# Kernel tuning notes

Measured on AMD Instinct MI355X. Metric: run time of the kernel, lower is better.

The kernel has to match this reference:

```python
import jax, jax.numpy as jnp
import numpy as np

B, C_IN, C_OUT, H, K = 64, 64, 128, 1855, 6


def setup_inputs() -> dict:
    key = jax.random.key(0)
    k1, k2, k3, k4 = jax.random.split(key, 4)
    x = jax.random.normal(k1, (B, C_IN, H), dtype=jnp.float32)
    # neighbor table [H, K]; valid indices first, -1 padding at the end
    neighbors = jax.random.randint(k2, (H, K), 0, H)
    n_boundary = H // 10
    neighbors = neighbors.at[:n_boundary, K - 2:].set(-1)
    weight_center = jax.random.normal(k3, (C_OUT, C_IN), dtype=jnp.float32) / np.sqrt(C_IN).astype(np.float32)
    weight_neighbors = jax.random.normal(k4, (C_OUT, C_IN, K), dtype=jnp.float32) / np.sqrt(C_IN * K).astype(np.float32)
    bias = jnp.zeros((C_OUT,), dtype=jnp.float32)
    return {
        "x": x,
        "neighbors": neighbors,
        "weight_center": weight_center,
        "weight_neighbors": weight_neighbors,
        "bias": bias,
    }


def reference(x, neighbors, weight_center, weight_neighbors, bias):
    # x: [B, C_in, H]; neighbors: [H, K] with -1 = invalid (valid-first ordering)
    mask = neighbors >= 0                               # [H, K]
    idx = jnp.where(mask, neighbors, 0)                 # safe gather indices
    gathered = x[:, :, idx] * mask.astype(x.dtype)[None, None, :, :]  # [B, C_in, H, K]
    center = jnp.einsum('bch,oc->boh', x, weight_center)              # [B, C_out, H]
    neigh = jnp.einsum('bchk,ock->boh', gathered, weight_neighbors)   # [B, C_out, H]
    counts = (1 + mask.sum(axis=-1)).astype(x.dtype)                  # [H]
    return (center + neigh) / counts[None, None, :] + bias[None, :, None]
```

## Files before the change

### kernel.cpp

```cpp
#include <hip/hip_runtime.h>
#include <stdint.h>

typedef __bf16 bf16x8 __attribute__((ext_vector_type(8)));
typedef float floatx4 __attribute__((ext_vector_type(4)));
typedef float floatx4u __attribute__((ext_vector_type(4), aligned(4)));
typedef unsigned int u32x4 __attribute__((ext_vector_type(4)));
typedef unsigned short u16;
typedef unsigned int u32;

#define CIN   64
#define COUT  128
#define H_    1855
#define KNB   6
#define KTOT  448
#define NSTEPS 14

#define HROW   2064
#define HBUFSZ 33024

#define WP_OFF     ((size_t)H_ * 4096 * 2)
#define CINV_OFF   (WP_OFF + (size_t)COUT * KTOT * 2)
#define ZERO_OFF   (CINV_OFF + 7424)
#define SRCOFF_OFF (ZERO_OFF + 1024)
#define INVOFF 0xFFFFFFFFu

#define PIN4(v) asm volatile("" : "+v"(v))

typedef __attribute__((address_space(1))) unsigned int as1_u32;
typedef __attribute__((address_space(3))) unsigned int as3_u32;
static __device__ __forceinline__ void ld16_to_lds(const void* g, void* l) {
    __builtin_amdgcn_global_load_lds((const as1_u32*)g, (as3_u32*)l, 16, 0, 0);
}

static __device__ inline u16 f32_to_bf16(float f) {
    u32 u = __float_as_uint(f);
    u32 r = (u + 0x7FFFu + ((u >> 16) & 1u)) >> 16;
    return (u16)r;
}

__global__ __launch_bounds__(256) void k_prep(const float* __restrict__ x,
                                              const float* __restrict__ wc,
                                              const float* __restrict__ wn,
                                              const int* __restrict__ nbr,
                                              u16* __restrict__ xt3,
                                              u16* __restrict__ wp,
                                              float* __restrict__ cInvG,
                                              u32* __restrict__ zeroPg,
                                              u32* __restrict__ srcOff) {
    int tid = threadIdx.x;
    if (blockIdx.y == 64) {
        for (int tg = blockIdx.x * 256 + tid; tg < COUT * KTOT; tg += 29 * 256) {
            if (tg < 128) zeroPg[tg] = 0u;
            if (tg < H_) {
                int cnt = 1;
#pragma unroll
                for (int j = 0; j < KNB; ++j) cnt += (nbr[tg * KNB + j] >= 0) ? 1 : 0;
                cInvG[tg] = 1.0f / (float)cnt;
            }
            if (tg < H_ * 8) {
                int h = tg >> 3, s = tg & 7;
                u32 e;
                if (s == 0) e = (u32)h * 8192u;
                else if (s <= 6) {
                    int n = nbr[h * KNB + (s - 1)];
                    e = (n >= 0) ? (u32)n * 8192u : INVOFF;
                } else e = INVOFF;
                srcOff[tg] = e;
            }
            int o = tg / KTOT;
            int rem = tg - o * KTOT;
            int s = rem >> 6, c = rem & 63;
            float v = (s == 0) ? wc[o * CIN + c]
                               : wn[(o * CIN + c) * KNB + (s - 1)];
            wp[tg] = f32_to_bf16(v);
        }
        return;
    }
    __shared__ u32 t32[64][34];
    int h0  = blockIdx.x * 64;
    int bc0 = blockIdx.y * 64;
    int lh = tid & 15;
    int rq = tid >> 4;
    bool safe = (h0 + 64 <= H_);
#pragma unroll
    for (int it = 0; it < 2; ++it) {
        int rp = it * 16 + rq;
        size_t r0 = (size_t)(bc0 + rp * 2) * H_;
        size_t r1 = r0 + H_;
        int h = h0 + lh * 4;
        u32 p[4];
        if (safe) {
            floatx4u f0 = *(const floatx4u*)(x + r0 + h);
            floatx4u f1 = *(const floatx4u*)(x + r1 + h);
#pragma unroll
            for (int j = 0; j < 4; ++j)
                p[j] = (u32)f32_to_bf16(f0[j]) | ((u32)f32_to_bf16(f1[j]) << 16);
        } else {
#pragma unroll
            for (int j = 0; j < 4; ++j) {
                int hh = h + j;
                u16 a = 0, b = 0;
                if (hh < H_) { a = f32_to_bf16(x[r0 + hh]); b = f32_to_bf16(x[r1 + hh]); }
                p[j] = (u32)a | ((u32)b << 16);
            }
        }
#pragma unroll
        for (int j = 0; j < 4; ++j) t32[lh * 4 + j][rp] = p[j];
    }
    __syncthreads();
    int bg = tid & 7;
    int hb = tid >> 3;
#pragma unroll
    for (int ii = 0; ii < 2; ++ii) {
        int hl = ii * 32 + hb;
        int hh = h0 + hl;
        uint2 qa = *(const uint2*)&t32[hl][bg * 4];
        uint2 qb = *(const uint2*)&t32[hl][bg * 4 + 2];
        u32x4 q = {qa.x, qa.y, qb.x, qb.y};
        if (hh < H_)
            *(u32x4*)(xt3 + (size_t)hh * 4096 + bc0 + bg * 8) = q;
    }
}

__global__ __launch_bounds__(256, 2) void k_main(const u16* __restrict__ xt3,
                                                 const u16* __restrict__ wp,
                                                 const float* __restrict__ bias,
                                                 const float* __restrict__ cInvG,
                                                 const u32* __restrict__ srcOff,
                                                 float* __restrict__ out) {
    __shared__ __align__(16) char LDS[2 * HBUFSZ];

    int tid  = threadIdx.x;
    int gbl  = blockIdx.x;
    int bq   = gbl & 15;
    int hs   = gbl >> 4;
    int b0   = bq * 4;
    int h0   = hs * 64;

    int lane = tid & 63;
    int wave = tid >> 6;
    int col  = lane & 15;
    int quad = lane >> 4;
    int m0w  = wave * 32;
    int lane16 = lane & 15;
    int ssub = lane >> 4;
    int bl   = lane16 >> 3;
    int chunk = lane16 & 7;

    const char* xb = (const char*)xt3;

    u32x4 afrag[2][NSTEPS];
#pragma unroll
    for (int mt = 0; mt < 2; ++mt) {
        int o = m0w + mt * 16 + col;
#pragma unroll
        for (int kk = 0; kk < NSTEPS; ++kk)
            afrag[mt][kk] = *(const u32x4*)(wp + o * KTOT + kk * 32 + quad * 8);
    }
#pragma unroll
    for (int mt = 0; mt < 2; ++mt)
#pragma unroll
        for (int kk = 0; kk < NSTEPS; ++kk)
            PIN4(afrag[mt][kk]);

    float biasv[2][4];
#pragma unroll
    for (int mt = 0; mt < 2; ++mt)
#pragma unroll
        for (int r = 0; r < 4; ++r)
            biasv[mt][r] = bias[m0w + mt * 16 + quad * 4 + r];

    float icv[4];
#pragma unroll
    for (int t = 0; t < 4; ++t) {
        int hic = h0 + t * 16 + col;
        icv[t] = cInvG[hic < H_ ? hic : 0];
    }

    u32 colOff = (u32)((b0 + bl) * 128 + chunk * 16);
    u32 zOff   = (u32)ZERO_OFF + (u32)(lane16 * 16);
    u32 offs[4][2][4];
#pragma unroll
    for (int t = 0; t < 4; ++t)
#pragma unroll
        for (int hf = 0; hf < 2; ++hf)
#pragma unroll
            for (int i = 0; i < 4; ++i) {
                int hh = h0 + t * 16 + wave * 4 + i;
                int s  = hf * 4 + ssub;
                u32 e = (hh < H_) ? srcOff[hh * 8 + s] : INVOFF;
                offs[t][hf][i] = (e == INVOFF) ? zOff : (e + colOff);
            }

    int rb = col * HROW + quad * 16;
    char* buf0 = LDS;
    char* buf1 = LDS + HBUFSZ;
    bool bnd = (hs == 28);

#define SGH(t, hf, bufp) do {                                                 \
    _Pragma("unroll")                                                         \
    for (int _j = 0; _j < 8; ++_j) {                                          \
        int _hl = _j >> 1, _bh = _j & 1;                                      \
        ld16_to_lds(xb + offs[t][hf][_hl] + _bh * 256,                        \
                    (bufp) + (wave * 4 + _hl) * HROW + _bh * 1024);           \
    }                                                                         \
} while (0)

#define CA(accv, bufp) do {              \
    _Pragma("unroll") for (int _m = 0; _m < 2; ++_m)                          \
    _Pragma("unroll") for (int _n = 0; _n < 4; ++_n)                          \
        accv[_m][_n] = (floatx4){0.0f, 0.0f, 0.0f, 0.0f};                     \
    __builtin_amdgcn_s_setprio(1);                                            \
    _Pragma("unroll")                                                         \
    for (int kk = 0; kk < 8; ++kk) {                                          \
        int _ko = (kk >> 1) * 256 + (kk & 1) * 64;                            \
        bf16x8 a0 = __builtin_bit_cast(bf16x8, afrag[0][kk]);                 \
        bf16x8 a1 = __builtin_bit_cast(bf16x8, afrag[1][kk]);                 \
        _Pragma("unroll")                                                     \
        for (int _n = 0; _n < 4; ++_n) {                                      \
            bf16x8 bf = *(const bf16x8*)((bufp) + rb + (_n >> 1) * 1024       \
                                         + (_n & 1) * 128 + _ko);             \
            accv[0][_n] = __builtin_amdgcn_mfma_f32_16x16x32_bf16(a0, bf, accv[0][_n], 0, 0, 0); \
            accv[1][_n] = __builtin_amdgcn_mfma_f32_16x16x32_bf16(a1, bf, accv[1][_n], 0, 0, 0); \
        }                                                                     \
    }                                                                         \
    __builtin_amdgcn_s_setprio(0);                                            \
} while (0)

#define CB(accv, bufp) do {            \
    __builtin_amdgcn_s_setprio(1);                                            \
    _Pragma("unroll")                                                         \
    for (int kk = 8; kk < 14; ++kk) {                                         \
        int _k2 = kk - 8;                                                     \
        int _ko = (_k2 >> 1) * 256 + (_k2 & 1) * 64;                          \
        bf16x8 a0 = __builtin_bit_cast(bf16x8, afrag[0][kk]);                 \
        bf16x8 a1 = __builtin_bit_cast(bf16x8, afrag[1][kk]);                 \
        _Pragma("unroll")                                                     \
        for (int _n = 0; _n < 4; ++_n) {                                      \
            bf16x8 bf = *(const bf16x8*)((bufp) + rb + (_n >> 1) * 1024       \
                                         + (_n & 1) * 128 + _ko);             \
            accv[0][_n] = __builtin_amdgcn_mfma_f32_16x16x32_bf16(a0, bf, accv[0][_n], 0, 0, 0); \
            accv[1][_n] = __builtin_amdgcn_mfma_f32_16x16x32_bf16(a1, bf, accv[1][_n], 0, 0, 0); \
        }                                                                     \
    }                                                                         \
    __builtin_amdgcn_s_setprio(0);                                            \
} while (0)

#define EPI(t, accv, BND) do {                                                \
    int _h = h0 + (t) * 16 + col;                                             \
    float _ic = icv[t];                                                       \
    bool _hv = !(BND) || (_h < H_);                                           \
    _Pragma("unroll") for (int _n = 0; _n < 4; ++_n)                          \
    _Pragma("unroll") for (int _m = 0; _m < 2; ++_m)                          \
    _Pragma("unroll") for (int _r = 0; _r < 4; ++_r) {                        \
        int _o = m0w + _m * 16 + quad * 4 + _r;                               \
        float _v = accv[_m][_n][_r] * _ic + biasv[_m][_r];                    \
        if (_hv) out[(size_t)(b0 + _n) * ((size_t)COUT * H_)                  \
                     + (size_t)_o * H_ + _h] = _v;                            \
    }                                                                         \
} while (0)

#define VW(n)  asm volatile("s_waitcnt vmcnt(" #n ") lgkmcnt(0)" ::: "memory")
#define BAR()  __builtin_amdgcn_s_barrier()

    floatx4 acc[2][4];

    SGH(0, 0, buf0);
    VW(0);  BAR(); SGH(0, 1, buf1); CA(acc, buf0);
    VW(0);  BAR(); SGH(1, 0, buf0); CB(acc, buf1);
    EPI(0, acc, false);
    VW(32); BAR(); SGH(1, 1, buf1); CA(acc, buf0);
    VW(0);  BAR(); SGH(2, 0, buf0); CB(acc, buf1);
    EPI(1, acc, false);
    VW(32); BAR(); SGH(2, 1, buf1); CA(acc, buf0);
    VW(0);  BAR(); SGH(3, 0, buf0); CB(acc, buf1);
    EPI(2, acc, false);
    VW(32); BAR(); SGH(3, 1, buf1); CA(acc, buf0);
    VW(0);  BAR();                  CB(acc, buf1);
    EPI(3, acc, bnd);

#undef SGH
#undef CA
#undef CB
#undef EPI
#undef VW
#undef BAR
}

extern "C" void kernel_launch(void* const* d_in, const int* in_sizes, int n_in,
                              void* d_out, int out_size, void* d_ws, size_t ws_size,
                              hipStream_t stream) {
    const float* x    = (const float*)d_in[0];
    const int*   nbr  = (const int*)d_in[1];
    const float* wc   = (const float*)d_in[2];
    const float* wn   = (const float*)d_in[3];
    const float* bias = (const float*)d_in[4];

    u16*   xt3    = (u16*)d_ws;
    u16*   wp     = (u16*)((char*)d_ws + WP_OFF);
    float* cInvG  = (float*)((char*)d_ws + CINV_OFF);
    u32*   zeroPg = (u32*)((char*)d_ws + ZERO_OFF);
    u32*   srcOff = (u32*)((char*)d_ws + SRCOFF_OFF);

    k_prep<<<dim3(29, 65), dim3(256), 0, stream>>>(
        x, wc, wn, nbr, xt3, wp, cInvG, zeroPg, srcOff);
    k_main<<<dim3(464), dim3(256), 0, stream>>>(
        xt3, wp, bias, cInvG, srcOff, (float*)d_out);
}
```

Before: 144.1 us.

## Split main kernel into smaller tiles over batch and output-channel halves

Each block of the main kernel now covers 2 batches and 64 output channels instead of 4 batches and 128. The grid grows from 464 to 1856 blocks, the LDS footprint and register use per block shrink, and occupancy rises to 4 blocks per CU. The neighbor offset table is staged into LDS per block instead of held in registers. Invalid neighbors now point at a zeroed row in the workspace instead of being special-cased in the kernel. Each block gathers more redundantly (the same x rows are fetched by both output-channel halves), and each MFMA weight fragment is reused across fewer batch columns.

```diff
diff --git a/kernel.cpp b/kernel.cpp
--- a/kernel.cpp
+++ b/kernel.cpp
@@ -15,14 +15,14 @@
 #define KTOT  448
 #define NSTEPS 14
 
-#define HROW   2064
-#define HBUFSZ 33024
+#define HROW   1040
+#define HBUFSZ 16640
+#define STAB_OFF (2 * HBUFSZ)
 
 #define WP_OFF     ((size_t)H_ * 4096 * 2)
 #define CINV_OFF   (WP_OFF + (size_t)COUT * KTOT * 2)
-#define ZERO_OFF   (CINV_OFF + 7424)
-#define SRCOFF_OFF (ZERO_OFF + 1024)
-#define INVOFF 0xFFFFFFFFu
+#define SRCOFF_OFF (CINV_OFF + 7424)
+#define ZROW_OFF   (SRCOFF_OFF + 59392)
 
 #define PIN4(v) asm volatile("" : "+v"(v))
 
@@ -45,12 +45,12 @@
                                               u16* __restrict__ xt3,
                                               u16* __restrict__ wp,
                                               float* __restrict__ cInvG,
-                                              u32* __restrict__ zeroPg,
-                                              u32* __restrict__ srcOff) {
+                                              u32* __restrict__ srcOff2,
+                                              u32* __restrict__ zrow) {
     int tid = threadIdx.x;
     if (blockIdx.y == 64) {
         for (int tg = blockIdx.x * 256 + tid; tg < COUT * KTOT; tg += 29 * 256) {
-            if (tg < 128) zeroPg[tg] = 0u;
+            if (tg < 2048) zrow[tg] = 0u;
             if (tg < H_) {
                 int cnt = 1;
 #pragma unroll
@@ -63,9 +63,9 @@
                 if (s == 0) e = (u32)h * 8192u;
                 else if (s <= 6) {
                     int n = nbr[h * KNB + (s - 1)];
-                    e = (n >= 0) ? (u32)n * 8192u : INVOFF;
-                } else e = INVOFF;
-                srcOff[tg] = e;
+                    e = (n >= 0) ? (u32)n * 8192u : (u32)ZROW_OFF;
+                } else e = (u32)ZROW_OFF;
+                srcOff2[tg] = e;
             }
             int o = tg / KTOT;
             int rem = tg - o * KTOT;
@@ -122,53 +122,59 @@
     }
 }
 
-__global__ __launch_bounds__(256, 2) void k_main(const u16* __restrict__ xt3,
+__global__ __launch_bounds__(256, 4) void k_main(const u16* __restrict__ xt3,
                                                  const u16* __restrict__ wp,
                                                  const float* __restrict__ bias,
                                                  const float* __restrict__ cInvG,
-                                                 const u32* __restrict__ srcOff,
+                                                 const u32* __restrict__ srcOff2,
                                                  float* __restrict__ out) {
-    __shared__ __align__(16) char LDS[2 * HBUFSZ];
+    __shared__ __align__(16) char LDS[2 * HBUFSZ + 2048];
 
     int tid  = threadIdx.x;
     int gbl  = blockIdx.x;
-    int bq   = gbl & 15;
-    int hs   = gbl >> 4;
-    int b0   = bq * 4;
+    int bp   = gbl & 31;
+    int rest = gbl >> 5;
+    int hs   = rest >> 1;
+    int om   = rest & 1;
+    int b0   = bp * 2;
     int h0   = hs * 64;
+    int om0  = om * 64;
 
     int lane = tid & 63;
     int wave = tid >> 6;
     int col  = lane & 15;
     int quad = lane >> 4;
-    int m0w  = wave * 32;
     int lane16 = lane & 15;
     int ssub = lane >> 4;
     int bl   = lane16 >> 3;
     int chunk = lane16 & 7;
+    int mrow = om0 + wave * 16;
 
     const char* xb = (const char*)xt3;
-
-    u32x4 afrag[2][NSTEPS];
-#pragma unroll
-    for (int mt = 0; mt < 2; ++mt) {
-        int o = m0w + mt * 16 + col;
+    u32* sTab = (u32*)(LDS + STAB_OFF);
+
+    {
+        int j0 = tid * 2;
+        int g0 = h0 * 8 + j0;
+        u32 e0 = (g0 < H_ * 8) ? srcOff2[g0] : (u32)ZROW_OFF;
+        u32 e1 = (g0 + 1 < H_ * 8) ? srcOff2[g0 + 1] : (u32)ZROW_OFF;
+        sTab[j0] = e0;
+        sTab[j0 + 1] = e1;
+    }
+
+    u32x4 afrag[NSTEPS];
+    {
+        int o = mrow + col;
 #pragma unroll
         for (int kk = 0; kk < NSTEPS; ++kk)
-            afrag[mt][kk] = *(const u32x4*)(wp + o * KTOT + kk * 32 + quad * 8);
-    }
-#pragma unroll
-    for (int mt = 0; mt < 2; ++mt)
-#pragma unroll
-        for (int kk = 0; kk < NSTEPS; ++kk)
-            PIN4(afrag[mt][kk]);
-
-    float biasv[2][4];
-#pragma unroll
-    for (int mt = 0; mt < 2; ++mt)
-#pragma unroll
-        for (int r = 0; r < 4; ++r)
-            biasv[mt][r] = bias[m0w + mt * 16 + quad * 4 + r];
+            afrag[kk] = *(const u32x4*)(wp + o * KTOT + kk * 32 + quad * 8);
+    }
+#pragma unroll
+    for (int kk = 0; kk < NSTEPS; ++kk) PIN4(afrag[kk]);
+
+    float biasv[4];
+#pragma unroll
+    for (int r = 0; r < 4; ++r) biasv[r] = bias[mrow + quad * 4 + r];
 
     float icv[4];
 #pragma unroll
@@ -178,83 +184,61 @@
     }
 
     u32 colOff = (u32)((b0 + bl) * 128 + chunk * 16);
-    u32 zOff   = (u32)ZERO_OFF + (u32)(lane16 * 16);
-    u32 offs[4][2][4];
-#pragma unroll
-    for (int t = 0; t < 4; ++t)
-#pragma unroll
-        for (int hf = 0; hf < 2; ++hf)
-#pragma unroll
-            for (int i = 0; i < 4; ++i) {
-                int hh = h0 + t * 16 + wave * 4 + i;
-                int s  = hf * 4 + ssub;
-                u32 e = (hh < H_) ? srcOff[hh * 8 + s] : INVOFF;
-                offs[t][hf][i] = (e == INVOFF) ? zOff : (e + colOff);
-            }
-
     int rb = col * HROW + quad * 16;
     char* buf0 = LDS;
     char* buf1 = LDS + HBUFSZ;
     bool bnd = (hs == 28);
 
+    __syncthreads();
+
 #define SGH(t, hf, bufp) do {                                                 \
     _Pragma("unroll")                                                         \
-    for (int _j = 0; _j < 8; ++_j) {                                          \
-        int _hl = _j >> 1, _bh = _j & 1;                                      \
-        ld16_to_lds(xb + offs[t][hf][_hl] + _bh * 256,                        \
-                    (bufp) + (wave * 4 + _hl) * HROW + _bh * 1024);           \
-    }                                                                         \
-} while (0)
-
-#define CA(accv, bufp) do {              \
-    _Pragma("unroll") for (int _m = 0; _m < 2; ++_m)                          \
-    _Pragma("unroll") for (int _n = 0; _n < 4; ++_n)                          \
-        accv[_m][_n] = (floatx4){0.0f, 0.0f, 0.0f, 0.0f};                     \
+    for (int _i = 0; _i < 4; ++_i) {                                          \
+        int _hl = wave * 4 + _i;                                              \
+        u32 _e = sTab[((t) * 16 + _hl) * 8 + (hf) * 4 + ssub];                \
+        ld16_to_lds(xb + _e + colOff, (bufp) + _hl * HROW);                   \
+    }                                                                         \
+} while (0)
+
+#define CA(bufp) do {                    \
+    acc[0] = (floatx4){0.0f, 0.0f, 0.0f, 0.0f};                               \
+    acc[1] = (floatx4){0.0f, 0.0f, 0.0f, 0.0f};                               \
     __builtin_amdgcn_s_setprio(1);                                            \
     _Pragma("unroll")                                                         \
     for (int kk = 0; kk < 8; ++kk) {                                          \
         int _ko = (kk >> 1) * 256 + (kk & 1) * 64;                            \
-        bf16x8 a0 = __builtin_bit_cast(bf16x8, afrag[0][kk]);                 \
-        bf16x8 a1 = __builtin_bit_cast(bf16x8, afrag[1][kk]);                 \
-        _Pragma("unroll")                                                     \
-        for (int _n = 0; _n < 4; ++_n) {                                      \
-            bf16x8 bf = *(const bf16x8*)((bufp) + rb + (_n >> 1) * 1024       \
-                                         + (_n & 1) * 128 + _ko);             \
-            accv[0][_n] = __builtin_amdgcn_mfma_f32_16x16x32_bf16(a0, bf, accv[0][_n], 0, 0, 0); \
-            accv[1][_n] = __builtin_amdgcn_mfma_f32_16x16x32_bf16(a1, bf, accv[1][_n], 0, 0, 0); \
-        }                                                                     \
+        bf16x8 bfa = *(const bf16x8*)((bufp) + rb + _ko);                     \
+        bf16x8 bfb = *(const bf16x8*)((bufp) + rb + 128 + _ko);               \
+        bf16x8 a = __builtin_bit_cast(bf16x8, afrag[kk]);                     \
+        acc[0] = __builtin_amdgcn_mfma_f32_16x16x32_bf16(a, bfa, acc[0], 0, 0, 0); \
+        acc[1] = __builtin_amdgcn_mfma_f32_16x16x32_bf16(a, bfb, acc[1], 0, 0, 0); \
     }                                                                         \
     __builtin_amdgcn_s_setprio(0);                                            \
 } while (0)
 
-#define CB(accv, bufp) do {            \
+#define CB(bufp) do {                  \
     __builtin_amdgcn_s_setprio(1);                                            \
     _Pragma("unroll")                                                         \
     for (int kk = 8; kk < 14; ++kk) {                                         \
         int _k2 = kk - 8;                                                     \
         int _ko = (_k2 >> 1) * 256 + (_k2 & 1) * 64;                          \
-        bf16x8 a0 = __builtin_bit_cast(bf16x8, afrag[0][kk]);                 \
-        bf16x8 a1 = __builtin_bit_cast(bf16x8, afrag[1][kk]);                 \
-        _Pragma("unroll")                                                     \
-        for (int _n = 0; _n < 4; ++_n) {                                      \
-            bf16x8 bf = *(const bf16x8*)((bufp) + rb + (_n >> 1) * 1024       \
-                                         + (_n & 1) * 128 + _ko);             \
-            accv[0][_n] = __builtin_amdgcn_mfma_f32_16x16x32_bf16(a0, bf, accv[0][_n], 0, 0, 0); \
-            accv[1][_n] = __builtin_amdgcn_mfma_f32_16x16x32_bf16(a1, bf, accv[1][_n], 0, 0, 0); \
-        }                                                                     \
+        bf16x8 bfa = *(const bf16x8*)((bufp) + rb + _ko);                     \
+        bf16x8 bfb = *(const bf16x8*)((bufp) + rb + 128 + _ko);               \
+        bf16x8 a = __builtin_bit_cast(bf16x8, afrag[kk]);                     \
+        acc[0] = __builtin_amdgcn_mfma_f32_16x16x32_bf16(a, bfa, acc[0], 0, 0, 0); \
+        acc[1] = __builtin_amdgcn_mfma_f32_16x16x32_bf16(a, bfb, acc[1], 0, 0, 0); \
     }                                                                         \
     __builtin_amdgcn_s_setprio(0);                                            \
 } while (0)
 
-#define EPI(t, accv, BND) do {                                                \
+#define EPI(t, BND) do {                                                      \
     int _h = h0 + (t) * 16 + col;                                             \
     float _ic = icv[t];                                                       \
     bool _hv = !(BND) || (_h < H_);                                           \
-    _Pragma("unroll") for (int _n = 0; _n < 4; ++_n)                          \
-    _Pragma("unroll") for (int _m = 0; _m < 2; ++_m)                          \
+    _Pragma("unroll") for (int _n = 0; _n < 2; ++_n)                          \
     _Pragma("unroll") for (int _r = 0; _r < 4; ++_r) {                        \
-        int _o = m0w + _m * 16 + quad * 4 + _r;                               \
-        float _v = accv[_m][_n][_r] * _ic + biasv[_m][_r];                    \
+        int _o = mrow + quad * 4 + _r;                                        \
+        float _v = acc[_n][_r] * _ic + biasv[_r];                             \
         if (_hv) out[(size_t)(b0 + _n) * ((size_t)COUT * H_)                  \
                      + (size_t)_o * H_ + _h] = _v;                            \
     }                                                                         \
@@ -263,21 +247,21 @@
 #define VW(n)  asm volatile("s_waitcnt vmcnt(" #n ") lgkmcnt(0)" ::: "memory")
 #define BAR()  __builtin_amdgcn_s_barrier()
 
-    floatx4 acc[2][4];
+    floatx4 acc[2];
 
     SGH(0, 0, buf0);
-    VW(0);  BAR(); SGH(0, 1, buf1); CA(acc, buf0);
-    VW(0);  BAR(); SGH(1, 0, buf0); CB(acc, buf1);
-    EPI(0, acc, false);
-    VW(32); BAR(); SGH(1, 1, buf1); CA(acc, buf0);
-    VW(0);  BAR(); SGH(2, 0, buf0); CB(acc, buf1);
-    EPI(1, acc, false);
-    VW(32); BAR(); SGH(2, 1, buf1); CA(acc, buf0);
-    VW(0);  BAR(); SGH(3, 0, buf0); CB(acc, buf1);
-    EPI(2, acc, false);
-    VW(32); BAR(); SGH(3, 1, buf1); CA(acc, buf0);
-    VW(0);  BAR();                  CB(acc, buf1);
-    EPI(3, acc, bnd);
+    VW(0); BAR(); SGH(0, 1, buf1); CA(buf0);
+    VW(0); BAR(); SGH(1, 0, buf0); CB(buf1);
+    EPI(0, false);
+    VW(8); BAR(); SGH(1, 1, buf1); CA(buf0);
+    VW(0); BAR(); SGH(2, 0, buf0); CB(buf1);
+    EPI(1, false);
+    VW(8); BAR(); SGH(2, 1, buf1); CA(buf0);
+    VW(0); BAR(); SGH(3, 0, buf0); CB(buf1);
+    EPI(2, false);
+    VW(8); BAR(); SGH(3, 1, buf1); CA(buf0);
+    VW(0); BAR();                  CB(buf1);
+    EPI(3, bnd);
 
 #undef SGH
 #undef CA
@@ -299,11 +283,11 @@
     u16*   xt3    = (u16*)d_ws;
     u16*   wp     = (u16*)((char*)d_ws + WP_OFF);
     float* cInvG  = (float*)((char*)d_ws + CINV_OFF);
-    u32*   zeroPg = (u32*)((char*)d_ws + ZERO_OFF);
     u32*   srcOff = (u32*)((char*)d_ws + SRCOFF_OFF);
+    u32*   zrow   = (u32*)((char*)d_ws + ZROW_OFF);
 
     k_prep<<<dim3(29, 65), dim3(256), 0, stream>>>(
-        x, wc, wn, nbr, xt3, wp, cInvG, zeroPg, srcOff);
-    k_main<<<dim3(464), dim3(256), 0, stream>>>(
+        x, wc, wn, nbr, xt3, wp, cInvG, srcOff, zrow);
+    k_main<<<dim3(1856), dim3(256), 0, stream>>>(
         xt3, wp, bias, cInvG, srcOff, (float*)d_out);
 }
```

New measurement: 141.7 us. No clear change (-1.6%).
